# Kernel tuning notes

Measured on AMD Instinct MI355X. Metric: run time of the kernel, lower is better.

## Reference

```python
import itertools
import jax, jax.numpy as jnp
import numpy as np

N_OBJECTS = 32
GRAPHLET_SIZE = 3
N_FILTERS = 16
REL_DIM = 16
BATCH = 32
N_GROUP_QUERIES = 512
BETA = 1.0

# static combinatorial groups: all C(32,3) = 4960 index triples
GROUP_IDX = jnp.asarray(
    np.array(list(itertools.combinations(range(N_OBJECTS), GRAPHLET_SIZE)), dtype=np.int32)
)  # (G, g)


def setup_inputs() -> dict:
    key = jax.random.key(0)
    k1, k2, k3 = jax.random.split(key, 3)
    inputs = jax.random.normal(k1, (BATCH, N_OBJECTS, N_OBJECTS, REL_DIM), dtype=jnp.float32)
    group_logits = jax.random.normal(k2, (N_GROUP_QUERIES, N_OBJECTS), dtype=jnp.float32)
    filters = jax.random.normal(k3, (N_FILTERS, GRAPHLET_SIZE, GRAPHLET_SIZE, REL_DIM), dtype=jnp.float32)
    return {"inputs": inputs, "group_logits": group_logits, "filters": filters}


def reference(inputs, group_logits, filters):
    idx = GROUP_IDX  # (G, g)
    # gather sub-relation tensors for every group in one fused advanced-index:
    # (B, G, g, g, D)
    sub_rel = inputs[:, idx[:, :, None], idx[:, None, :], :]
    # relational inner product with all filters: (B, G, F)
    rel_conv = jnp.einsum('bgijd,fijd->bgf', sub_rel, filters)
    # soft group weights
    sp = jax.nn.softplus(group_logits)            # (Gi, N)
    group_obj_w = sp[:, idx]                      # (Gi, G, g) -- gather along object axis
    group_w = jnp.prod(group_obj_w, axis=-1)      # (Gi, G)
    norm_w = jax.nn.softmax(BETA * group_w, axis=-1)  # (Gi, G)
    # contract over combinatorial groups: (B, Gi, F)
    out = jnp.einsum('bnr,gn->bgr', rel_conv, norm_w)
    return out
```

## Files before the change

kernel.cpp:

```cpp
#include <hip/hip_runtime.h>
#include <hip/hip_bf16.h>

#define N_OBJ   32
#define G_TOTAL 4960
#define NPAIR   496
#define KTOT    1600
#define SEG01   0
#define SEG02   496
#define SEG12   992
#define SEGD0   1488
#define SEGD1   1520
#define SEGD2   1552
#define N_FILT  16
#define REL_D   16
#define BATCH   32
#define NQ      512
#define ZSPLIT  10
#define KCH     160
#define NIT     5

typedef __attribute__((ext_vector_type(8))) short bf16x8;
typedef __attribute__((ext_vector_type(4))) float f32x4;

static __device__ inline unsigned short f2bf(float x) {
    union { float f; unsigned int u; } v; v.f = x;
    unsigned int r = v.u + 0x7fffu + ((v.u >> 16) & 1u);
    return (unsigned short)(r >> 16);
}
static __device__ inline void gload_lds16(const void* g, void* l) {
    __builtin_amdgcn_global_load_lds(
        (const __attribute__((address_space(1))) unsigned int*)g,
        (__attribute__((address_space(3))) unsigned int*)(unsigned int)(uintptr_t)l,
        16, 0, 0);
}
static __device__ inline int pbase(int x) { return (x * (63 - x)) >> 1; }
static __device__ inline void unrank2(int u, int& x, int& y) {
    for (x = 0; x < 31; x++) { int len = 31 - x; if (u < len) break; u -= len; }
    y = x + 1 + u;
}
static __device__ inline float dot16(float4 a0, float4 a1, float4 a2, float4 a3,
                                     const float* F) {
    float4 f0 = *(const float4*)(F);
    float4 f1 = *(const float4*)(F + 4);
    float4 f2 = *(const float4*)(F + 8);
    float4 f3 = *(const float4*)(F + 12);
    float d = a0.x * f0.x + a0.y * f0.y + a0.z * f0.z + a0.w * f0.w;
    d += a1.x * f1.x + a1.y * f1.y + a1.z * f1.z + a1.w * f1.w;
    d += a2.x * f2.x + a2.y * f2.y + a2.z * f2.z + a2.w * f2.w;
    d += a3.x * f3.x + a3.y * f3.y + a3.z * f3.z + a3.w * f3.w;
    return d;
}

__global__ __launch_bounds__(1024) void k_front(const float* __restrict__ logits,
                                                const float* __restrict__ inputs,
                                                const float* __restrict__ filters,
                                                unsigned short* __restrict__ Wp,
                                                unsigned short* __restrict__ Bp) {
    __shared__ __align__(16) char smem[11648];
    int t = threadIdx.x;
    int role = blockIdx.x;

    if (role < NQ) {
        float* sp  = (float*)smem;
        float* red = (float*)(smem + 128);
        float* Wf  = (float*)(smem + 192);
        int q = role;
        if (t < N_OBJ) {
            float x = logits[q * N_OBJ + t];
            float ex = __expf(x);
            sp[t] = (x > 15.f) ? x : __logf(1.f + ex);
        }
        __syncthreads();

#pragma unroll
        for (int rep = 0; rep < 2; rep++) {
            int idx = t + rep * 1024;
            if (idx < 3 * NPAIR) {
                int which = idx / NPAIR;
                int u = idx - which * NPAIR;
                int x, y; unrank2(u, x, y);
                float pxy = sp[x] * sp[y];
                int lo, hi;
                if (which == 0)      { lo = y + 1; hi = 32; }
                else if (which == 1) { lo = x + 1; hi = y;  }
                else                 { lo = 0;     hi = x;  }
                const float4* sp4 = (const float4*)sp;
                float s = 0.f;
#pragma unroll
                for (int cb = 0; cb < 8; cb++) {
                    float4 v = sp4[cb];
                    int c0 = cb * 4;
                    s += (c0 + 0 >= lo && c0 + 0 < hi) ? __expf(pxy * v.x) : 0.f;
                    s += (c0 + 1 >= lo && c0 + 1 < hi) ? __expf(pxy * v.y) : 0.f;
                    s += (c0 + 2 >= lo && c0 + 2 < hi) ? __expf(pxy * v.z) : 0.f;
                    s += (c0 + 3 >= lo && c0 + 3 < hi) ? __expf(pxy * v.w) : 0.f;
                }
                Wf[which * NPAIR + u] = s;
            }
        }
        __syncthreads();

        if (t < 512) {
            float lsum = (t < NPAIR) ? Wf[t] : 0.f;
#pragma unroll
            for (int off = 32; off; off >>= 1) lsum += __shfl_down(lsum, off, 64);
            if ((t & 63) == 0) red[t >> 6] = lsum;
        } else if (t < 608) {
            int which = (t - 512) >> 5, idx = t & 31;
            float s = 0.f;
            if (which == 0) {
                int base = pbase(idx);
                for (int u = idx + 1; u < 32; u++) s += Wf[SEG01 + base + u - idx - 1];
                Wf[SEGD0 + idx] = s;
            } else if (which == 1) {
                for (int a2 = 0; a2 < idx; a2++) s += Wf[SEG01 + pbase(a2) + idx - a2 - 1];
                Wf[SEGD1 + idx] = s;
            } else {
                for (int b2 = 0; b2 < idx; b2++) s += Wf[SEG12 + pbase(b2) + idx - b2 - 1];
                Wf[SEGD2 + idx] = s;
            }
        } else if (t < 624) {
            Wf[1584 + (t - 608)] = 0.f;
        }
        __syncthreads();

        if (t < KTOT / 2) {
            float total = red[0] + red[1] + red[2] + red[3] +
                          red[4] + red[5] + red[6] + red[7];
            float inv = 1.f / total;
            unsigned int pk = (unsigned int)f2bf(Wf[2 * t] * inv) |
                              ((unsigned int)f2bf(Wf[2 * t + 1] * inv) << 16);
            ((unsigned int*)(Wp + (size_t)q * KTOT))[t] = pk;
        }
    } else {
        float* flt = (float*)smem;
        int role2 = role - NQ;
        if (t < 576) {
            int i4 = t * 4;
            int f = i4 / 144;
            int r = i4 - f * 144;
            *(float4*)&flt[f * 180 + (r >> 4) * 20 + (r & 15)] = *(const float4*)(filters + i4);
        }
        __syncthreads();

        int oldbid = role2 * 4 + (t >> 8);
        int tp = t & 255;
        int b = oldbid / 9, ch = oldbid - b * 9;
        int lane = tp & 63, fq = tp >> 6;
        int u = ch * 64 + lane;
        if (u < NPAIR) {
            int x, y; unrank2(u, x, y);
            const float4* rxy = (const float4*)(inputs + (((size_t)b * 32 + x) * 32 + y) * 16);
            const float4* ryx = (const float4*)(inputs + (((size_t)b * 32 + y) * 32 + x) * 16);
            float4 a0 = rxy[0], a1 = rxy[1], a2 = rxy[2], a3 = rxy[3];
            float4 c0 = ryx[0], c1 = ryx[1], c2 = ryx[2], c3 = ryx[3];
#pragma unroll
            for (int fi = 0; fi < 4; fi++) {
                const float* F = &flt[(fq * 4 + fi) * 180];
                float v01 = dot16(a0, a1, a2, a3, F + 1 * 20) + dot16(c0, c1, c2, c3, F + 3 * 20);
                float v02 = dot16(a0, a1, a2, a3, F + 2 * 20) + dot16(c0, c1, c2, c3, F + 6 * 20);
                float v12 = dot16(a0, a1, a2, a3, F + 5 * 20) + dot16(c0, c1, c2, c3, F + 7 * 20);
                size_t nrow = ((size_t)b * 16 + fq * 4 + fi) * KTOT;
                Bp[nrow + SEG01 + u] = f2bf(v01);
                Bp[nrow + SEG02 + u] = f2bf(v02);
                Bp[nrow + SEG12 + u] = f2bf(v12);
            }
        } else if (u < 528) {
            int x = u - NPAIR;
            const float4* rxx = (const float4*)(inputs + (((size_t)b * 32 + x) * 32 + x) * 16);
            float4 a0 = rxx[0], a1 = rxx[1], a2 = rxx[2], a3 = rxx[3];
#pragma unroll
            for (int fi = 0; fi < 4; fi++) {
                const float* F = &flt[(fq * 4 + fi) * 180];
                float v0 = dot16(a0, a1, a2, a3, F + 0 * 20);
                float v4 = dot16(a0, a1, a2, a3, F + 4 * 20);
                float v8 = dot16(a0, a1, a2, a3, F + 8 * 20);
                size_t nrow = ((size_t)b * 16 + fq * 4 + fi) * KTOT;
                Bp[nrow + SEGD0 + x] = f2bf(v0);
                Bp[nrow + SEGD1 + x] = f2bf(v4);
                Bp[nrow + SEGD2 + x] = f2bf(v8);
            }
        } else if (ch == 8 && lane >= 16 && lane < 32) {
            int col = lane - 16;
#pragma unroll
            for (int fi = 0; fi < 4; fi++)
                Bp[((size_t)b * 16 + fq * 4 + fi) * KTOT + 1584 + col] = 0;
        }
    }
}

__global__ __launch_bounds__(256) void k_gemm(const unsigned short* __restrict__ A,
                                              const unsigned short* __restrict__ Bm,
                                              float* __restrict__ part) {
    __shared__ __align__(16) unsigned short As[2][64 * 32];
    __shared__ __align__(16) unsigned short Bs[2][64 * 32];
    int tid = threadIdx.x;
    int q0 = blockIdx.x * 64, n0 = blockIdx.y * 64, z = blockIdx.z;
    int k0 = z * KCH;
    int wave = tid >> 6, lane = tid & 63;
    int wm = wave & 1, wn = wave >> 1;
    int row16 = lane & 15, quad = lane >> 4;

    int srow = tid >> 2;
    int schunk = (tid & 3) ^ ((srow >> 1) & 3);
    const unsigned short* ga = A + (size_t)(q0 + srow) * KTOT + k0 + schunk * 8;
    const unsigned short* gb = Bm + (size_t)(n0 + srow) * KTOT + k0 + schunk * 8;
    char* lA = (char*)&As[0][0] + tid * 16;
    char* lB = (char*)&Bs[0][0] + tid * 16;

    f32x4 acc[2][2] = {};
    int fchunk = (quad ^ ((row16 >> 1) & 3)) * 8;

    gload_lds16(ga, lA);
    gload_lds16(gb, lB);
    for (int it = 0; it < NIT; ++it) {
        __syncthreads();
        if (it + 1 < NIT) {
            int nb = (it + 1) & 1;
            gload_lds16(ga + (it + 1) * 32, lA + nb * 64 * 32 * 2);
            gload_lds16(gb + (it + 1) * 32, lB + nb * 64 * 32 * 2);
        }
        int buf = it & 1;
        bf16x8 afr[2], bfr[2];
#pragma unroll
        for (int mi = 0; mi < 2; mi++)
            afr[mi] = *(const bf16x8*)&As[buf][(wm * 32 + mi * 16 + row16) * 32 + fchunk];
#pragma unroll
        for (int ni = 0; ni < 2; ni++)
            bfr[ni] = *(const bf16x8*)&Bs[buf][(wn * 32 + ni * 16 + row16) * 32 + fchunk];
#pragma unroll
        for (int mi = 0; mi < 2; mi++)
#pragma unroll
            for (int ni = 0; ni < 2; ni++)
                acc[mi][ni] = __builtin_amdgcn_mfma_f32_16x16x32_bf16(
                    afr[mi], bfr[ni], acc[mi][ni], 0, 0, 0);
    }

    float* pz = part + (size_t)z * (NQ * 512);
#pragma unroll
    for (int mi = 0; mi < 2; mi++)
#pragma unroll
        for (int ni = 0; ni < 2; ni++)
#pragma unroll
            for (int r = 0; r < 4; r++) {
                int q = q0 + wm * 32 + mi * 16 + quad * 4 + r;
                int n = n0 + wn * 32 + ni * 16 + row16;
                pz[q * 512 + n] = acc[mi][ni][r];
            }
}

__global__ __launch_bounds__(256) void k_reduce(const float* __restrict__ part,
                                                float* __restrict__ out) {
    int gid = blockIdx.x * 256 + threadIdx.x;
    int q = gid >> 7;
    int n = (gid & 127) * 4;
    float4 a = *(const float4*)(part + q * 512 + n);
#pragma unroll
    for (int zz = 1; zz < ZSPLIT; zz++) {
        float4 b4 = *(const float4*)(part + (size_t)zz * (NQ * 512) + q * 512 + n);
        a.x += b4.x; a.y += b4.y; a.z += b4.z; a.w += b4.w;
    }
    *(float4*)(out + (size_t)(n >> 4) * (NQ * REL_D) + q * 16 + (n & 15)) = a;
}

extern "C" void kernel_launch(void* const* d_in, const int* in_sizes, int n_in,
                              void* d_out, int out_size, void* d_ws, size_t ws_size,
                              hipStream_t stream) {
    const float* inputs  = (const float*)d_in[0];
    const float* logits  = (const float*)d_in[1];
    const float* filters = (const float*)d_in[2];
    float* out = (float*)d_out;

    char* ws = (char*)d_ws;
    unsigned short* Wp = (unsigned short*)ws;
    unsigned short* Bp = (unsigned short*)(ws + 1638400);
    float*          part = (float*)(ws + 3276800);

    k_front<<<NQ + 72, 1024, 0, stream>>>(logits, inputs, filters, Wp, Bp);
    k_gemm<<<dim3(8, 8, ZSPLIT), 256, 0, stream>>>(Wp, Bp, part);
    k_reduce<<<NQ * 512 / 4 / 256, 256, 0, stream>>>(part, out);
}
```

Measured before the change: 80.90 us.

## Replace split-K GEMM plus reduce with smaller-tile full-K GEMM writing output directly

The split-K GEMM (64x64 tiles, 10 K-chunks) and its separate reduction kernel are replaced by one GEMM using 32x32 output tiles over the full K of 1600, in 64-wide steps with a swizzled LDS layout. Each wave computes one 16x16 MFMA tile and stores straight to the output. This removes the partial-sum buffer round-trip and one kernel launch. In exchange there are 256 blocks with a long serial K loop, one MFMA chain per wave and lower operand reuse per tile.

```diff
diff --git a/kernel.cpp b/kernel.cpp
--- a/kernel.cpp
+++ b/kernel.cpp
@@ -15,9 +15,7 @@
 #define REL_D   16
 #define BATCH   32
 #define NQ      512
-#define ZSPLIT  10
-#define KCH     160
-#define NIT     5
+#define NIT2    25
 
 typedef __attribute__((ext_vector_type(8))) short bf16x8;
 typedef __attribute__((ext_vector_type(4))) float f32x4;
@@ -191,76 +189,51 @@
 
 __global__ __launch_bounds__(256) void k_gemm(const unsigned short* __restrict__ A,
                                               const unsigned short* __restrict__ Bm,
-                                              float* __restrict__ part) {
-    __shared__ __align__(16) unsigned short As[2][64 * 32];
-    __shared__ __align__(16) unsigned short Bs[2][64 * 32];
+                                              float* __restrict__ out) {
+    __shared__ __align__(16) unsigned short As[2][32 * 64];
+    __shared__ __align__(16) unsigned short Bs[2][32 * 64];
     int tid = threadIdx.x;
-    int q0 = blockIdx.x * 64, n0 = blockIdx.y * 64, z = blockIdx.z;
-    int k0 = z * KCH;
+    int q0 = blockIdx.x * 32, n0 = blockIdx.y * 32;
     int wave = tid >> 6, lane = tid & 63;
     int wm = wave & 1, wn = wave >> 1;
     int row16 = lane & 15, quad = lane >> 4;
 
-    int srow = tid >> 2;
-    int schunk = (tid & 3) ^ ((srow >> 1) & 3);
-    const unsigned short* ga = A + (size_t)(q0 + srow) * KTOT + k0 + schunk * 8;
-    const unsigned short* gb = Bm + (size_t)(n0 + srow) * KTOT + k0 + schunk * 8;
+    int srow = tid >> 3;
+    int schunk = (tid & 7) ^ ((srow >> 1) & 7);
+    const unsigned short* ga = A + (size_t)(q0 + srow) * KTOT + schunk * 8;
+    const unsigned short* gb = Bm + (size_t)(n0 + srow) * KTOT + schunk * 8;
     char* lA = (char*)&As[0][0] + tid * 16;
     char* lB = (char*)&Bs[0][0] + tid * 16;
 
-    f32x4 acc[2][2] = {};
-    int fchunk = (quad ^ ((row16 >> 1) & 3)) * 8;
+    f32x4 acc = {};
+    int xk = (row16 >> 1) & 7;
 
     gload_lds16(ga, lA);
     gload_lds16(gb, lB);
-    for (int it = 0; it < NIT; ++it) {
-        __syncthreads();
-        if (it + 1 < NIT) {
+    for (int it = 0; it < NIT2; ++it) {
+        __syncthreads();
+        if (it + 1 < NIT2) {
             int nb = (it + 1) & 1;
-            gload_lds16(ga + (it + 1) * 32, lA + nb * 64 * 32 * 2);
-            gload_lds16(gb + (it + 1) * 32, lB + nb * 64 * 32 * 2);
+            gload_lds16(ga + (it + 1) * 64, lA + nb * 32 * 64 * 2);
+            gload_lds16(gb + (it + 1) * 64, lB + nb * 32 * 64 * 2);
         }
         int buf = it & 1;
-        bf16x8 afr[2], bfr[2];
-#pragma unroll
-        for (int mi = 0; mi < 2; mi++)
-            afr[mi] = *(const bf16x8*)&As[buf][(wm * 32 + mi * 16 + row16) * 32 + fchunk];
-#pragma unroll
-        for (int ni = 0; ni < 2; ni++)
-            bfr[ni] = *(const bf16x8*)&Bs[buf][(wn * 32 + ni * 16 + row16) * 32 + fchunk];
-#pragma unroll
-        for (int mi = 0; mi < 2; mi++)
-#pragma unroll
-            for (int ni = 0; ni < 2; ni++)
-                acc[mi][ni] = __builtin_amdgcn_mfma_f32_16x16x32_bf16(
-                    afr[mi], bfr[ni], acc[mi][ni], 0, 0, 0);
+#pragma unroll
+        for (int ks = 0; ks < 2; ks++) {
+            int ca = (((ks * 4) + quad) ^ xk) * 8;
+            bf16x8 afr = *(const bf16x8*)&As[buf][(wm * 16 + row16) * 64 + ca];
+            bf16x8 bfr = *(const bf16x8*)&Bs[buf][(wn * 16 + row16) * 64 + ca];
+            acc = __builtin_amdgcn_mfma_f32_16x16x32_bf16(afr, bfr, acc, 0, 0, 0);
+        }
     }
 
-    float* pz = part + (size_t)z * (NQ * 512);
-#pragma unroll
-    for (int mi = 0; mi < 2; mi++)
-#pragma unroll
-        for (int ni = 0; ni < 2; ni++)
-#pragma unroll
-            for (int r = 0; r < 4; r++) {
-                int q = q0 + wm * 32 + mi * 16 + quad * 4 + r;
-                int n = n0 + wn * 32 + ni * 16 + row16;
-                pz[q * 512 + n] = acc[mi][ni][r];
-            }
-}
-
-__global__ __launch_bounds__(256) void k_reduce(const float* __restrict__ part,
-                                                float* __restrict__ out) {
-    int gid = blockIdx.x * 256 + threadIdx.x;
-    int q = gid >> 7;
-    int n = (gid & 127) * 4;
-    float4 a = *(const float4*)(part + q * 512 + n);
-#pragma unroll
-    for (int zz = 1; zz < ZSPLIT; zz++) {
-        float4 b4 = *(const float4*)(part + (size_t)zz * (NQ * 512) + q * 512 + n);
-        a.x += b4.x; a.y += b4.y; a.z += b4.z; a.w += b4.w;
+    int bq = (n0 + wn * 16) >> 4;
+    float* o = out + (size_t)bq * (NQ * REL_D) + row16;
+#pragma unroll
+    for (int r = 0; r < 4; r++) {
+        int q = q0 + wm * 16 + quad * 4 + r;
+        o[q * REL_D] = acc[r];
     }
-    *(float4*)(out + (size_t)(n >> 4) * (NQ * REL_D) + q * 16 + (n & 15)) = a;
 }
 
 extern "C" void kernel_launch(void* const* d_in, const int* in_sizes, int n_in,
@@ -274,9 +247,7 @@
     char* ws = (char*)d_ws;
     unsigned short* Wp = (unsigned short*)ws;
     unsigned short* Bp = (unsigned short*)(ws + 1638400);
-    float*          part = (float*)(ws + 3276800);
 
     k_front<<<NQ + 72, 1024, 0, stream>>>(logits, inputs, filters, Wp, Bp);
-    k_gemm<<<dim3(8, 8, ZSPLIT), 256, 0, stream>>>(Wp, Bp, part);
-    k_reduce<<<NQ * 512 / 4 / 256, 256, 0, stream>>>(part, out);
-}
+    k_gemm<<<dim3(16, 16), 256, 0, stream>>>(Wp, Bp, out);
+}
```

Result: no change. 81.91 us (+1.2%).
